# Kernel optimization log

Measured on AMD Instinct MI355X. Metric: run time of the kernel, lower is better.

## Reference

```python
import jax, jax.numpy as jnp
import numpy as np

S = 16          # slice count (init kwarg)
EPS = 1e-5      # BN2d default eps


def markov_sub(m, s):
    """Vectorized get_markov_sub. m: [C, C] -> [s, C, C].
    ms[i][a,b] = where(m[i,b] > 0, m[a,b], 0); mss[k] = max over rows i in slice k.
    Equivalent closed form via per-column any/all positivity of the slice rows."""
    C = m.shape[0]
    pos = (m > 0.0).reshape(s, C // s, C)          # [s, slice_size, C]
    any_p = pos.any(axis=1)[:, None, :]            # [s, 1, C]
    all_p = pos.all(axis=1)[:, None, :]            # [s, 1, C]
    mb = m[None, :, :]                             # [1, C, C]
    return jnp.where(all_p, mb,
                     jnp.where(any_p, jnp.maximum(mb, 0.0), jnp.zeros_like(mb)))


def setup_inputs() -> dict:
    key = jax.random.key(0)
    ks = jax.random.split(key, 8)
    N, C, H, W = 4, 256, 32, 32
    s = S
    feats = jax.random.normal(ks[0], (N, C, H, W), jnp.float32)
    adj_matrix = jax.random.normal(ks[1], (N, C, C), jnp.float32)
    # three 1x1 conv layers: in = S*C, out = C (stacked on leading axis)
    conv_w = jax.random.normal(ks[2], (3, C, s * C), jnp.float32) / np.sqrt(s * C).astype(np.float32)
    conv_b = jax.random.normal(ks[3], (3, C), jnp.float32) * 0.01
    bn_gamma = jnp.ones((3, C), jnp.float32)
    bn_beta = jnp.zeros((3, C), jnp.float32)
    bn_mean = jax.random.normal(ks[4], (3, C), jnp.float32) * 0.1
    bn_var = jax.random.uniform(ks[5], (3, C), jnp.float32, minval=0.5, maxval=1.5)
    return {"feats": feats, "adj_matrix": adj_matrix, "conv_w": conv_w,
            "conv_b": conv_b, "bn_gamma": bn_gamma, "bn_beta": bn_beta,
            "bn_mean": bn_mean, "bn_var": bn_var}


def reference(feats, adj_matrix, conv_w, conv_b, bn_gamma, bn_beta, bn_mean, bn_var):
    N, C, H, W = feats.shape
    s = S
    # per-sample markov sub-adjacencies, computed once and reused across layers
    mss = jax.vmap(lambda m: markov_sub(m, s))(adj_matrix)      # [N, S, C, C]
    mss = mss.reshape(N, s * C, C)                              # [N, S*C, C]
    outs = []
    x = feats
    for l in range(3):
        xp = x.reshape(N, C, H * W)                             # [N, C, HW]
        y = jnp.einsum('nkc,ncp->nkp', mss, xp)                 # sparse.mm -> [N, S*C, HW]
        y = jnp.einsum('ok,nkp->nop', conv_w[l], y) + conv_b[l][None, :, None]
        scale = (bn_gamma[l] * jax.lax.rsqrt(bn_var[l] + EPS))[None, :, None]
        y = (y - bn_mean[l][None, :, None]) * scale + bn_beta[l][None, :, None]
        y = jax.nn.relu(y).reshape(N, C, H, W)
        outs.append(y)
        x = y
    return tuple(outs)
```

## Files before the change

kernel.cpp:

```cpp
#include <hip/hip_runtime.h>
#include <stdint.h>

#define CC   256
#define NB   4
#define HWP  1024
#define EPSV 1e-5f

typedef __attribute__((ext_vector_type(8))) short bf16x8;
typedef __attribute__((ext_vector_type(4))) float f32x4;

__device__ __forceinline__ ushort f2bf(float f) {
    uint32_t u = __float_as_uint(f);
    uint32_t r = (u + 0x7FFFu + ((u >> 16) & 1u)) >> 16;
    return (ushort)r;
}

__global__ __launch_bounds__(256) void prep_kernel(const float* __restrict__ adj,
                                                   const float* __restrict__ conv_w,
                                                   ushort* __restrict__ mpT,
                                                   uint8_t* __restrict__ flags,
                                                   ushort* __restrict__ cwS) {
    const int t = threadIdx.x;
    if (blockIdx.x < 64) {
        const int bb = blockIdx.x;
        const int n = bb >> 4;
        const int at = (bb >> 2) & 3, bt = bb & 3;
        const int a0 = at * 64, b0 = bt * 64;
        const float* m = adj + (size_t)n * CC * CC;
        __shared__ float Ms[64][68];
        {
            const int ar = t >> 2, bq = (t & 3) * 16;
            const float* src = m + (size_t)(a0 + ar) * CC + b0 + bq;
#pragma unroll
            for (int i = 0; i < 4; ++i)
                *(float4*)&Ms[ar][bq + i * 4] = *(const float4*)(src + i * 4);
        }
        __syncthreads();
        {
            const int bl = t >> 2, ac = (t & 3) * 16;
            ushort* dst = mpT + ((size_t)n * CC + b0 + bl) * CC + a0 + ac;
#pragma unroll
            for (int a4 = 0; a4 < 4; ++a4) {
                ushort4 o;
                o.x = f2bf(fmaxf(Ms[ac + a4 * 4 + 0][bl], 0.f));
                o.y = f2bf(fmaxf(Ms[ac + a4 * 4 + 1][bl], 0.f));
                o.z = f2bf(fmaxf(Ms[ac + a4 * 4 + 2][bl], 0.f));
                o.w = f2bf(fmaxf(Ms[ac + a4 * 4 + 3][bl], 0.f));
                *(ushort4*)(dst + a4 * 4) = o;
            }
        }
        {
            const int kl = t >> 6, bl = t & 63;
            bool allp = true, anyp = false;
#pragma unroll
            for (int i = 0; i < 16; ++i) {
                bool p = Ms[kl * 16 + i][bl] > 0.0f;
                allp = allp && p;
                anyp = anyp || p;
            }
            const uint8_t f = allp ? (uint8_t)2 : (anyp ? (uint8_t)1 : (uint8_t)0);
            flags[(((size_t)n * CC) + b0 + bl) * 16 + at * 4 + kl] = f;
        }
    } else {
        const int idx = ((blockIdx.x - 64) * 256 + t) * 4;
        const float* src = conv_w + ((size_t)(idx >> 8)) * 4096 + (idx & 255);
        float4 s = {0.f, 0.f, 0.f, 0.f};
#pragma unroll
        for (int k = 0; k < 16; ++k) {
            float4 v = *(const float4*)(src + k * 256);
            s.x += v.x; s.y += v.y; s.z += v.z; s.w += v.w;
        }
        ushort4 ob = {f2bf(s.x), f2bf(s.y), f2bf(s.z), f2bf(s.w)};
        *(ushort4*)(cwS + idx) = ob;
    }
}

__global__ __launch_bounds__(256) void wbase_mfma(const ushort* __restrict__ cwS,
                                                  const ushort* __restrict__ mpT,
                                                  const uint8_t* __restrict__ flags,
                                                  const float* __restrict__ adj,
                                                  const float* __restrict__ conv_w,
                                                  const float* __restrict__ gamma,
                                                  const float* __restrict__ var,
                                                  ushort* __restrict__ Ws) {
    const int tile = blockIdx.x;
    const int ln = blockIdx.y;
    const int l = ln >> 2, n = ln & 3;
    const int trow = (tile >> 2) * 64, tcol = (tile & 3) * 64;
    const ushort* A = cwS + (size_t)l * 65536;
    const ushort* B = mpT + (size_t)n * 65536;
    __shared__ ushort Al[64][40];
    __shared__ ushort Bl[64][40];
    __shared__ int   s_badcnt;
    __shared__ int   s_bad[1024];
    __shared__ float s_v[256];
    __shared__ float s_corr[64];
    const int t = threadIdx.x;
    const int wv = t >> 6, L = t & 63;
    const int wr = (wv >> 1) * 32, wc = (wv & 1) * 32;
    const int l16 = L & 15, q = L >> 4;
    const int r0 = t >> 2, kq0 = (t & 3) * 8;
    f32x4 acc[2][2];
#pragma unroll
    for (int i = 0; i < 2; ++i)
#pragma unroll
        for (int j = 0; j < 2; ++j)
            acc[i][j] = (f32x4){0.f, 0.f, 0.f, 0.f};

    if (t == 0) s_badcnt = 0;

    for (int kt = 0; kt < 8; ++kt) {
        const int kk = kt * 32;
        int4 av = *(const int4*)(A + (size_t)(trow + r0) * CC + kk + kq0);
        int4 bv = *(const int4*)(B + (size_t)(tcol + r0) * CC + kk + kq0);
        __syncthreads();
        *(int4*)&Al[r0][kq0] = av;
        *(int4*)&Bl[r0][kq0] = bv;
        __syncthreads();
        bf16x8 af[2], bfr[2];
#pragma unroll
        for (int i = 0; i < 2; ++i)
            af[i] = *(const bf16x8*)&Al[wr + i * 16 + l16][q * 8];
#pragma unroll
        for (int j = 0; j < 2; ++j)
            bfr[j] = *(const bf16x8*)&Bl[wc + j * 16 + l16][q * 8];
#pragma unroll
        for (int i = 0; i < 2; ++i)
#pragma unroll
            for (int j = 0; j < 2; ++j)
                acc[i][j] = __builtin_amdgcn_mfma_f32_16x16x32_bf16(af[i], bfr[j], acc[i][j], 0, 0, 0);
    }

    if (t < 64) {
        const uint8_t* fb = flags + (((size_t)n * CC) + tcol + t) * 16;
        const uint4 fv = *(const uint4*)fb;
        if ((fv.x != 0x01010101u) || (fv.y != 0x01010101u) ||
            (fv.z != 0x01010101u) || (fv.w != 0x01010101u)) {
            for (int k = 0; k < 16; ++k) {
                const int f = fb[k];
                if (f != 1) {
                    int pos = atomicAdd(&s_badcnt, 1);
                    s_bad[pos] = (t << 8) | (k << 2) | f;
                }
            }
        }
    }
    __syncthreads();
    const int nbad = s_badcnt;
    for (int e = 0; e < nbad; ++e) {
        const int enc = s_bad[e];
        const int bl = enc >> 8, k = (enc >> 2) & 15, f = enc & 3;
        const int b = tcol + bl;
        {
            const float mv = adj[(size_t)n * 65536 + (size_t)t * CC + b];
            s_v[t] = (f == 0) ? fmaxf(mv, 0.f) : fmaxf(-mv, 0.f);
        }
        __syncthreads();
        {
            const float* cw = conv_w + (size_t)l * 1048576 +
                              (size_t)(trow + (t >> 2)) * 4096 + k * 256 + (t & 3) * 64;
            const float* vv = s_v + (t & 3) * 64;
            float s = 0.f;
#pragma unroll 16
            for (int a = 0; a < 64; ++a) s += cw[a] * vv[a];
            s += __shfl_xor(s, 1);
            s += __shfl_xor(s, 2);
            if ((t & 3) == 0) s_corr[t >> 2] = s;
        }
        __syncthreads();
#pragma unroll
        for (int j = 0; j < 2; ++j) {
            if (wc + j * 16 + l16 == bl) {
#pragma unroll
                for (int i = 0; i < 2; ++i)
#pragma unroll
                    for (int r = 0; r < 4; ++r)
                        acc[i][j][r] -= s_corr[wr + i * 16 + q * 4 + r];
            }
        }
        __syncthreads();
    }

    ushort* W = Ws + (size_t)ln * 65536;
#pragma unroll
    for (int i = 0; i < 2; ++i)
#pragma unroll
        for (int j = 0; j < 2; ++j) {
            const int ob = trow + wr + i * 16 + q * 4;
            const int b  = tcol + wc + j * 16 + l16;
#pragma unroll
            for (int r = 0; r < 4; ++r) {
                const int o = ob + r;
                const float sc = gamma[l * CC + o] * rsqrtf(var[l * CC + o] + EPSV);
                W[(size_t)o * CC + b] = f2bf(acc[i][j][r] * sc);
            }
        }
}

__global__ __launch_bounds__(256) void fused_layers(const float* __restrict__ feats,
                                                    const ushort* __restrict__ Ws,
                                                    const float* __restrict__ conv_b,
                                                    const float* __restrict__ gamma,
                                                    const float* __restrict__ beta,
                                                    const float* __restrict__ mean,
                                                    const float* __restrict__ var,
                                                    float* __restrict__ out) {
    const int n = blockIdx.y;
    const int p0 = blockIdx.x * 16;
    __shared__ ushort xl[2][16][264];
    const int t = threadIdx.x;
    const int wv = t >> 6, L = t & 63;
    const int l16 = L & 15, q = L >> 4;

    {
        const float* src = feats + ((size_t)n * CC + t) * HWP + p0;
        float v[16];
#pragma unroll
        for (int i = 0; i < 4; ++i)
            *(float4*)&v[i * 4] = *(const float4*)(src + i * 4);
#pragma unroll
        for (int i = 0; i < 16; ++i)
            xl[0][i][t] = f2bf(v[i]);
    }
    __syncthreads();

    int cur = 0;
    for (int l = 0; l < 3; ++l) {
        const ushort* Bw = Ws + (size_t)(l * 4 + n) * 65536;
        f32x4 acc[4];
#pragma unroll
        for (int jj = 0; jj < 4; ++jj) acc[jj] = (f32x4){0.f, 0.f, 0.f, 0.f};

#pragma unroll
        for (int kt = 0; kt < 8; ++kt) {
            const int kk = kt * 32;
            bf16x8 af = *(const bf16x8*)&xl[cur][l16][kk + q * 8];
#pragma unroll
            for (int jj = 0; jj < 4; ++jj) {
                const int o = (wv * 4 + jj) * 16 + l16;
                bf16x8 bv = *(const bf16x8*)(Bw + (size_t)o * CC + kk + q * 8);
                acc[jj] = __builtin_amdgcn_mfma_f32_16x16x32_bf16(af, bv, acc[jj], 0, 0, 0);
            }
        }

        float* outn = out + (size_t)(l * 4 + n) * CC * HWP;
#pragma unroll
        for (int jj = 0; jj < 4; ++jj) {
            const int o = (wv * 4 + jj) * 16 + l16;
            const float sc = gamma[l * CC + o] * rsqrtf(var[l * CC + o] + EPSV);
            const float b2 = sc * (conv_b[l * CC + o] - mean[l * CC + o]) + beta[l * CC + o];
            const float v0 = fmaxf(acc[jj][0] + b2, 0.f);
            const float v1 = fmaxf(acc[jj][1] + b2, 0.f);
            const float v2 = fmaxf(acc[jj][2] + b2, 0.f);
            const float v3 = fmaxf(acc[jj][3] + b2, 0.f);
            *(float4*)(outn + (size_t)o * HWP + p0 + q * 4) = (float4){v0, v1, v2, v3};
            if (l < 2) {
                xl[cur ^ 1][q * 4 + 0][o] = f2bf(v0);
                xl[cur ^ 1][q * 4 + 1][o] = f2bf(v1);
                xl[cur ^ 1][q * 4 + 2][o] = f2bf(v2);
                xl[cur ^ 1][q * 4 + 3][o] = f2bf(v3);
            }
        }
        __syncthreads();
        cur ^= 1;
    }
}

extern "C" void kernel_launch(void* const* d_in, const int* in_sizes, int n_in,
                              void* d_out, int out_size, void* d_ws, size_t ws_size,
                              hipStream_t stream) {
    const float* feats  = (const float*)d_in[0];
    const float* adj    = (const float*)d_in[1];
    const float* conv_w = (const float*)d_in[2];
    const float* conv_b = (const float*)d_in[3];
    const float* gamma  = (const float*)d_in[4];
    const float* beta   = (const float*)d_in[5];
    const float* mean   = (const float*)d_in[6];
    const float* var    = (const float*)d_in[7];
    float* out = (float*)d_out;

    char* ws = (char*)d_ws;
    uint8_t* flags = (uint8_t*)ws;
    ushort*  cwS   = (ushort*)(ws + 16384);
    ushort*  mpT   = (ushort*)(ws + 409600);
    ushort*  Wsb   = (ushort*)(ws + 933888);

    prep_kernel<<<256, 256, 0, stream>>>(adj, conv_w, mpT, flags, cwS);
    wbase_mfma<<<dim3(16, 12), 256, 0, stream>>>(cwS, mpT, flags, adj, conv_w, gamma, var, Wsb);
    fused_layers<<<dim3(64, NB), 256, 0, stream>>>(feats, Wsb, conv_b, gamma, beta, mean, var, out);
}
```

Measured before the change: 114.3 us.

## Merge three kernels into one cooperative kernel with grid-wide syncs

```diff
diff --git a/kernel.cpp b/kernel.cpp
--- a/kernel.cpp
+++ b/kernel.cpp
@@ -1,5 +1,8 @@
 #include <hip/hip_runtime.h>
+#include <hip/hip_cooperative_groups.h>
 #include <stdint.h>
+
+namespace cg = cooperative_groups;
 
 #define CC   256
 #define NB   4
@@ -15,19 +18,35 @@
     return (ushort)r;
 }
 
-__global__ __launch_bounds__(256) void prep_kernel(const float* __restrict__ adj,
-                                                   const float* __restrict__ conv_w,
-                                                   ushort* __restrict__ mpT,
-                                                   uint8_t* __restrict__ flags,
-                                                   ushort* __restrict__ cwS) {
+__global__ __launch_bounds__(256) void mega_kernel(
+    const float* __restrict__ adj,   const float* __restrict__ conv_w,
+    const float* __restrict__ feats, const float* __restrict__ conv_b,
+    const float* __restrict__ gamma, const float* __restrict__ beta,
+    const float* __restrict__ mean,  const float* __restrict__ var,
+    float* __restrict__ out,
+    uint8_t* __restrict__ flags, ushort* __restrict__ cwS,
+    ushort* __restrict__ mpT,    ushort* __restrict__ Ws) {
+    cg::grid_group grid = cg::this_grid();
     const int t = threadIdx.x;
-    if (blockIdx.x < 64) {
-        const int bb = blockIdx.x;
-        const int n = bb >> 4;
-        const int at = (bb >> 2) & 3, bt = bb & 3;
+    const int bid = blockIdx.x;
+
+    __shared__ float  Ms[64][68];
+    __shared__ ushort Al[64][40];
+    __shared__ ushort Bl[64][40];
+    __shared__ int    s_badcnt;
+    __shared__ int    s_bad[1024];
+    __shared__ float  s_v[256];
+    __shared__ float  s_corr[64];
+    __shared__ ushort xl[2][16][264];
+
+    const int wv = t >> 6, L = t & 63;
+    const int l16 = L & 15, q = L >> 4;
+
+    if (bid < 64) {
+        const int n = bid >> 4;
+        const int at = (bid >> 2) & 3, bt = bid & 3;
         const int a0 = at * 64, b0 = bt * 64;
         const float* m = adj + (size_t)n * CC * CC;
-        __shared__ float Ms[64][68];
         {
             const int ar = t >> 2, bq = (t & 3) * 16;
             const float* src = m + (size_t)(a0 + ar) * CC + b0 + bq;
@@ -62,7 +81,7 @@
             flags[(((size_t)n * CC) + b0 + bl) * 16 + at * 4 + kl] = f;
         }
     } else {
-        const int idx = ((blockIdx.x - 64) * 256 + t) * 4;
+        const int idx = ((bid - 64) * 256 + t) * 4;
         const float* src = conv_w + ((size_t)(idx >> 8)) * 4096 + (idx & 255);
         float4 s = {0.f, 0.f, 0.f, 0.f};
 #pragma unroll
@@ -73,146 +92,8 @@
         ushort4 ob = {f2bf(s.x), f2bf(s.y), f2bf(s.z), f2bf(s.w)};
         *(ushort4*)(cwS + idx) = ob;
     }
-}
-
-__global__ __launch_bounds__(256) void wbase_mfma(const ushort* __restrict__ cwS,
-                                                  const ushort* __restrict__ mpT,
-                                                  const uint8_t* __restrict__ flags,
-                                                  const float* __restrict__ adj,
-                                                  const float* __restrict__ conv_w,
-                                                  const float* __restrict__ gamma,
-                                                  const float* __restrict__ var,
-                                                  ushort* __restrict__ Ws) {
-    const int tile = blockIdx.x;
-    const int ln = blockIdx.y;
-    const int l = ln >> 2, n = ln & 3;
-    const int trow = (tile >> 2) * 64, tcol = (tile & 3) * 64;
-    const ushort* A = cwS + (size_t)l * 65536;
-    const ushort* B = mpT + (size_t)n * 65536;
-    __shared__ ushort Al[64][40];
-    __shared__ ushort Bl[64][40];
-    __shared__ int   s_badcnt;
-    __shared__ int   s_bad[1024];
-    __shared__ float s_v[256];
-    __shared__ float s_corr[64];
-    const int t = threadIdx.x;
-    const int wv = t >> 6, L = t & 63;
-    const int wr = (wv >> 1) * 32, wc = (wv & 1) * 32;
-    const int l16 = L & 15, q = L >> 4;
-    const int r0 = t >> 2, kq0 = (t & 3) * 8;
-    f32x4 acc[2][2];
-#pragma unroll
-    for (int i = 0; i < 2; ++i)
-#pragma unroll
-        for (int j = 0; j < 2; ++j)
-            acc[i][j] = (f32x4){0.f, 0.f, 0.f, 0.f};
-
-    if (t == 0) s_badcnt = 0;
-
-    for (int kt = 0; kt < 8; ++kt) {
-        const int kk = kt * 32;
-        int4 av = *(const int4*)(A + (size_t)(trow + r0) * CC + kk + kq0);
-        int4 bv = *(const int4*)(B + (size_t)(tcol + r0) * CC + kk + kq0);
-        __syncthreads();
-        *(int4*)&Al[r0][kq0] = av;
-        *(int4*)&Bl[r0][kq0] = bv;
-        __syncthreads();
-        bf16x8 af[2], bfr[2];
-#pragma unroll
-        for (int i = 0; i < 2; ++i)
-            af[i] = *(const bf16x8*)&Al[wr + i * 16 + l16][q * 8];
-#pragma unroll
-        for (int j = 0; j < 2; ++j)
-            bfr[j] = *(const bf16x8*)&Bl[wc + j * 16 + l16][q * 8];
-#pragma unroll
-        for (int i = 0; i < 2; ++i)
-#pragma unroll
-            for (int j = 0; j < 2; ++j)
-                acc[i][j] = __builtin_amdgcn_mfma_f32_16x16x32_bf16(af[i], bfr[j], acc[i][j], 0, 0, 0);
-    }
-
-    if (t < 64) {
-        const uint8_t* fb = flags + (((size_t)n * CC) + tcol + t) * 16;
-        const uint4 fv = *(const uint4*)fb;
-        if ((fv.x != 0x01010101u) || (fv.y != 0x01010101u) ||
-            (fv.z != 0x01010101u) || (fv.w != 0x01010101u)) {
-            for (int k = 0; k < 16; ++k) {
-                const int f = fb[k];
-                if (f != 1) {
-                    int pos = atomicAdd(&s_badcnt, 1);
-                    s_bad[pos] = (t << 8) | (k << 2) | f;
-                }
-            }
-        }
-    }
-    __syncthreads();
-    const int nbad = s_badcnt;
-    for (int e = 0; e < nbad; ++e) {
-        const int enc = s_bad[e];
-        const int bl = enc >> 8, k = (enc >> 2) & 15, f = enc & 3;
-        const int b = tcol + bl;
-        {
-            const float mv = adj[(size_t)n * 65536 + (size_t)t * CC + b];
-            s_v[t] = (f == 0) ? fmaxf(mv, 0.f) : fmaxf(-mv, 0.f);
-        }
-        __syncthreads();
-        {
-            const float* cw = conv_w + (size_t)l * 1048576 +
-                              (size_t)(trow + (t >> 2)) * 4096 + k * 256 + (t & 3) * 64;
-            const float* vv = s_v + (t & 3) * 64;
-            float s = 0.f;
-#pragma unroll 16
-            for (int a = 0; a < 64; ++a) s += cw[a] * vv[a];
-            s += __shfl_xor(s, 1);
-            s += __shfl_xor(s, 2);
-            if ((t & 3) == 0) s_corr[t >> 2] = s;
-        }
-        __syncthreads();
-#pragma unroll
-        for (int j = 0; j < 2; ++j) {
-            if (wc + j * 16 + l16 == bl) {
-#pragma unroll
-                for (int i = 0; i < 2; ++i)
-#pragma unroll
-                    for (int r = 0; r < 4; ++r)
-                        acc[i][j][r] -= s_corr[wr + i * 16 + q * 4 + r];
-            }
-        }
-        __syncthreads();
-    }
-
-    ushort* W = Ws + (size_t)ln * 65536;
-#pragma unroll
-    for (int i = 0; i < 2; ++i)
-#pragma unroll
-        for (int j = 0; j < 2; ++j) {
-            const int ob = trow + wr + i * 16 + q * 4;
-            const int b  = tcol + wc + j * 16 + l16;
-#pragma unroll
-            for (int r = 0; r < 4; ++r) {
-                const int o = ob + r;
-                const float sc = gamma[l * CC + o] * rsqrtf(var[l * CC + o] + EPSV);
-                W[(size_t)o * CC + b] = f2bf(acc[i][j][r] * sc);
-            }
-        }
-}
-
-__global__ __launch_bounds__(256) void fused_layers(const float* __restrict__ feats,
-                                                    const ushort* __restrict__ Ws,
-                                                    const float* __restrict__ conv_b,
-                                                    const float* __restrict__ gamma,
-                                                    const float* __restrict__ beta,
-                                                    const float* __restrict__ mean,
-                                                    const float* __restrict__ var,
-                                                    float* __restrict__ out) {
-    const int n = blockIdx.y;
-    const int p0 = blockIdx.x * 16;
-    __shared__ ushort xl[2][16][264];
-    const int t = threadIdx.x;
-    const int wv = t >> 6, L = t & 63;
-    const int l16 = L & 15, q = L >> 4;
-
     {
+        const int n = bid >> 6, p0 = (bid & 63) * 16;
         const float* src = feats + ((size_t)n * CC + t) * HWP + p0;
         float v[16];
 #pragma unroll
@@ -222,56 +103,165 @@
         for (int i = 0; i < 16; ++i)
             xl[0][i][t] = f2bf(v[i]);
     }
-    __syncthreads();
-
-    int cur = 0;
-    for (int l = 0; l < 3; ++l) {
-        const ushort* Bw = Ws + (size_t)(l * 4 + n) * 65536;
-        f32x4 acc[4];
-#pragma unroll
-        for (int jj = 0; jj < 4; ++jj) acc[jj] = (f32x4){0.f, 0.f, 0.f, 0.f};
-
-#pragma unroll
+    grid.sync();
+
+    if (bid < 192) {
+        const int tile = bid & 15, ln = bid >> 4;
+        const int l = ln >> 2, n = ln & 3;
+        const int trow = (tile >> 2) * 64, tcol = (tile & 3) * 64;
+        const ushort* A = cwS + (size_t)l * 65536;
+        const ushort* B = mpT + (size_t)n * 65536;
+        const int wr = (wv >> 1) * 32, wc = (wv & 1) * 32;
+        const int r0 = t >> 2, kq0 = (t & 3) * 8;
+        f32x4 acc[2][2];
+#pragma unroll
+        for (int i = 0; i < 2; ++i)
+#pragma unroll
+            for (int j = 0; j < 2; ++j)
+                acc[i][j] = (f32x4){0.f, 0.f, 0.f, 0.f};
+
+        if (t == 0) s_badcnt = 0;
+
         for (int kt = 0; kt < 8; ++kt) {
             const int kk = kt * 32;
-            bf16x8 af = *(const bf16x8*)&xl[cur][l16][kk + q * 8];
+            int4 av = *(const int4*)(A + (size_t)(trow + r0) * CC + kk + kq0);
+            int4 bv = *(const int4*)(B + (size_t)(tcol + r0) * CC + kk + kq0);
+            __syncthreads();
+            *(int4*)&Al[r0][kq0] = av;
+            *(int4*)&Bl[r0][kq0] = bv;
+            __syncthreads();
+            bf16x8 af[2], bfr[2];
+#pragma unroll
+            for (int i = 0; i < 2; ++i)
+                af[i] = *(const bf16x8*)&Al[wr + i * 16 + l16][q * 8];
+#pragma unroll
+            for (int j = 0; j < 2; ++j)
+                bfr[j] = *(const bf16x8*)&Bl[wc + j * 16 + l16][q * 8];
+#pragma unroll
+            for (int i = 0; i < 2; ++i)
+#pragma unroll
+                for (int j = 0; j < 2; ++j)
+                    acc[i][j] = __builtin_amdgcn_mfma_f32_16x16x32_bf16(af[i], bfr[j], acc[i][j], 0, 0, 0);
+        }
+
+        if (t < 64) {
+            const uint8_t* fb = flags + (((size_t)n * CC) + tcol + t) * 16;
+            const uint4 fv = *(const uint4*)fb;
+            if ((fv.x != 0x01010101u) || (fv.y != 0x01010101u) ||
+                (fv.z != 0x01010101u) || (fv.w != 0x01010101u)) {
+                for (int k = 0; k < 16; ++k) {
+                    const int f = fb[k];
+                    if (f != 1) {
+                        int pos = atomicAdd(&s_badcnt, 1);
+                        s_bad[pos] = (t << 8) | (k << 2) | f;
+                    }
+                }
+            }
+        }
+        __syncthreads();
+        const int nbad = s_badcnt;
+        for (int e = 0; e < nbad; ++e) {
+            const int enc = s_bad[e];
+            const int bl = enc >> 8, k = (enc >> 2) & 15, f = enc & 3;
+            const int b = tcol + bl;
+            {
+                const float mv = adj[(size_t)n * 65536 + (size_t)t * CC + b];
+                s_v[t] = (f == 0) ? fmaxf(mv, 0.f) : fmaxf(-mv, 0.f);
+            }
+            __syncthreads();
+            {
+                const float* cw = conv_w + (size_t)l * 1048576 +
+                                  (size_t)(trow + (t >> 2)) * 4096 + k * 256 + (t & 3) * 64;
+                const float* vv = s_v + (t & 3) * 64;
+                float s = 0.f;
+#pragma unroll 16
+                for (int a = 0; a < 64; ++a) s += cw[a] * vv[a];
+                s += __shfl_xor(s, 1);
+                s += __shfl_xor(s, 2);
+                if ((t & 3) == 0) s_corr[t >> 2] = s;
+            }
+            __syncthreads();
+#pragma unroll
+            for (int j = 0; j < 2; ++j) {
+                if (wc + j * 16 + l16 == bl) {
+#pragma unroll
+                    for (int i = 0; i < 2; ++i)
+#pragma unroll
+                        for (int r = 0; r < 4; ++r)
+                            acc[i][j][r] -= s_corr[wr + i * 16 + q * 4 + r];
+                }
+            }
+            __syncthreads();
+        }
+
+        ushort* W = Ws + (size_t)ln * 65536;
+#pragma unroll
+        for (int i = 0; i < 2; ++i)
+#pragma unroll
+            for (int j = 0; j < 2; ++j) {
+                const int ob = trow + wr + i * 16 + q * 4;
+                const int b  = tcol + wc + j * 16 + l16;
+#pragma unroll
+                for (int r = 0; r < 4; ++r) {
+                    const int o = ob + r;
+                    const float sc = gamma[l * CC + o] * rsqrtf(var[l * CC + o] + EPSV);
+                    W[(size_t)o * CC + b] = f2bf(acc[i][j][r] * sc);
+                }
+            }
+    }
+    grid.sync();
+
+    {
+        const int n = bid >> 6, p0 = (bid & 63) * 16;
+        int cur = 0;
+        for (int l = 0; l < 3; ++l) {
+            const ushort* Bw = Ws + (size_t)(l * 4 + n) * 65536;
+            f32x4 acc[4];
+#pragma unroll
+            for (int jj = 0; jj < 4; ++jj) acc[jj] = (f32x4){0.f, 0.f, 0.f, 0.f};
+
+#pragma unroll
+            for (int kt = 0; kt < 8; ++kt) {
+                const int kk = kt * 32;
+                bf16x8 af = *(const bf16x8*)&xl[cur][l16][kk + q * 8];
+#pragma unroll
+                for (int jj = 0; jj < 4; ++jj) {
+                    const int o = (wv * 4 + jj) * 16 + l16;
+                    bf16x8 bv = *(const bf16x8*)(Bw + (size_t)o * CC + kk + q * 8);
+                    acc[jj] = __builtin_amdgcn_mfma_f32_16x16x32_bf16(af, bv, acc[jj], 0, 0, 0);
+                }
+            }
+
+            float* outn = out + (size_t)(l * 4 + n) * CC * HWP;
 #pragma unroll
             for (int jj = 0; jj < 4; ++jj) {
                 const int o = (wv * 4 + jj) * 16 + l16;
-                bf16x8 bv = *(const bf16x8*)(Bw + (size_t)o * CC + kk + q * 8);
-                acc[jj] = __builtin_amdgcn_mfma_f32_16x16x32_bf16(af, bv, acc[jj], 0, 0, 0);
-            }
-        }
-
-        float* outn = out + (size_t)(l * 4 + n) * CC * HWP;
-#pragma unroll
-        for (int jj = 0; jj < 4; ++jj) {
-            const int o = (wv * 4 + jj) * 16 + l16;
-            const float sc = gamma[l * CC + o] * rsqrtf(var[l * CC + o] + EPSV);
-            const float b2 = sc * (conv_b[l * CC + o] - mean[l * CC + o]) + beta[l * CC + o];
-            const float v0 = fmaxf(acc[jj][0] + b2, 0.f);
-            const float v1 = fmaxf(acc[jj][1] + b2, 0.f);
-            const float v2 = fmaxf(acc[jj][2] + b2, 0.f);
-            const float v3 = fmaxf(acc[jj][3] + b2, 0.f);
-            *(float4*)(outn + (size_t)o * HWP + p0 + q * 4) = (float4){v0, v1, v2, v3};
-            if (l < 2) {
-                xl[cur ^ 1][q * 4 + 0][o] = f2bf(v0);
-                xl[cur ^ 1][q * 4 + 1][o] = f2bf(v1);
-                xl[cur ^ 1][q * 4 + 2][o] = f2bf(v2);
-                xl[cur ^ 1][q * 4 + 3][o] = f2bf(v3);
-            }
-        }
-        __syncthreads();
-        cur ^= 1;
+                const float sc = gamma[l * CC + o] * rsqrtf(var[l * CC + o] + EPSV);
+                const float b2 = sc * (conv_b[l * CC + o] - mean[l * CC + o]) + beta[l * CC + o];
+                const float v0 = fmaxf(acc[jj][0] + b2, 0.f);
+                const float v1 = fmaxf(acc[jj][1] + b2, 0.f);
+                const float v2 = fmaxf(acc[jj][2] + b2, 0.f);
+                const float v3 = fmaxf(acc[jj][3] + b2, 0.f);
+                *(float4*)(outn + (size_t)o * HWP + p0 + q * 4) = (float4){v0, v1, v2, v3};
+                if (l < 2) {
+                    xl[cur ^ 1][q * 4 + 0][o] = f2bf(v0);
+                    xl[cur ^ 1][q * 4 + 1][o] = f2bf(v1);
+                    xl[cur ^ 1][q * 4 + 2][o] = f2bf(v2);
+                    xl[cur ^ 1][q * 4 + 3][o] = f2bf(v3);
+                }
+            }
+            __syncthreads();
+            cur ^= 1;
+        }
     }
 }
 
 extern "C" void kernel_launch(void* const* d_in, const int* in_sizes, int n_in,
                               void* d_out, int out_size, void* d_ws, size_t ws_size,
                               hipStream_t stream) {
-    const float* feats  = (const float*)d_in[0];
     const float* adj    = (const float*)d_in[1];
     const float* conv_w = (const float*)d_in[2];
+    const float* feats  = (const float*)d_in[0];
     const float* conv_b = (const float*)d_in[3];
     const float* gamma  = (const float*)d_in[4];
     const float* beta   = (const float*)d_in[5];
@@ -285,7 +275,8 @@
     ushort*  mpT   = (ushort*)(ws + 409600);
     ushort*  Wsb   = (ushort*)(ws + 933888);
 
-    prep_kernel<<<256, 256, 0, stream>>>(adj, conv_w, mpT, flags, cwS);
-    wbase_mfma<<<dim3(16, 12), 256, 0, stream>>>(cwS, mpT, flags, adj, conv_w, gamma, var, Wsb);
-    fused_layers<<<dim3(64, NB), 256, 0, stream>>>(feats, Wsb, conv_b, gamma, beta, mean, var, out);
+    void* args[] = {(void*)&adj, (void*)&conv_w, (void*)&feats, (void*)&conv_b,
+                    (void*)&gamma, (void*)&beta, (void*)&mean, (void*)&var,
+                    (void*)&out, (void*)&flags, (void*)&cwS, (void*)&mpT, (void*)&Wsb};
+    hipLaunchCooperativeKernel((void*)mega_kernel, dim3(256), dim3(256), args, 0, stream);
 }
```

Measured after the change: 173.2 us. 51.5% more time.

## Stage wbase K in two 128-wide halves and widen fused_layers to 512 threads

Applied to the files above, without the earlier changes.

```diff
diff --git a/kernel.cpp b/kernel.cpp
--- a/kernel.cpp
+++ b/kernel.cpp
@@ -89,8 +89,8 @@
     const int trow = (tile >> 2) * 64, tcol = (tile & 3) * 64;
     const ushort* A = cwS + (size_t)l * 65536;
     const ushort* B = mpT + (size_t)n * 65536;
-    __shared__ ushort Al[64][40];
-    __shared__ ushort Bl[64][40];
+    __shared__ ushort Al[64][130];
+    __shared__ ushort Bl[64][130];
     __shared__ int   s_badcnt;
     __shared__ int   s_bad[1024];
     __shared__ float s_v[256];
@@ -99,7 +99,7 @@
     const int wv = t >> 6, L = t & 63;
     const int wr = (wv >> 1) * 32, wc = (wv & 1) * 32;
     const int l16 = L & 15, q = L >> 4;
-    const int r0 = t >> 2, kq0 = (t & 3) * 8;
+    const int lr = t >> 2, lc0 = (t & 3) * 32;
     f32x4 acc[2][2];
 #pragma unroll
     for (int i = 0; i < 2; ++i)
@@ -109,21 +109,54 @@
 
     if (t == 0) s_badcnt = 0;
 
-    for (int kt = 0; kt < 8; ++kt) {
-        const int kk = kt * 32;
-        int4 av = *(const int4*)(A + (size_t)(trow + r0) * CC + kk + kq0);
-        int4 bv = *(const int4*)(B + (size_t)(tcol + r0) * CC + kk + kq0);
-        __syncthreads();
-        *(int4*)&Al[r0][kq0] = av;
-        *(int4*)&Bl[r0][kq0] = bv;
-        __syncthreads();
+    const ushort* Arow = A + (size_t)(trow + lr) * CC + lc0;
+    const ushort* Brow = B + (size_t)(tcol + lr) * CC + lc0;
+    int4 a1[4], b1[4], a2[4], b2[4];
+#pragma unroll
+    for (int j = 0; j < 4; ++j) a1[j] = *(const int4*)(Arow + j * 8);
+#pragma unroll
+    for (int j = 0; j < 4; ++j) b1[j] = *(const int4*)(Brow + j * 8);
+#pragma unroll
+    for (int j = 0; j < 4; ++j) {
+        *(int4*)&Al[lr][lc0 + j * 8] = a1[j];
+        *(int4*)&Bl[lr][lc0 + j * 8] = b1[j];
+    }
+    __syncthreads();
+#pragma unroll
+    for (int j = 0; j < 4; ++j) a2[j] = *(const int4*)(Arow + 128 + j * 8);
+#pragma unroll
+    for (int j = 0; j < 4; ++j) b2[j] = *(const int4*)(Brow + 128 + j * 8);
+#pragma unroll
+    for (int ktl = 0; ktl < 4; ++ktl) {
         bf16x8 af[2], bfr[2];
 #pragma unroll
         for (int i = 0; i < 2; ++i)
-            af[i] = *(const bf16x8*)&Al[wr + i * 16 + l16][q * 8];
+            af[i] = *(const bf16x8*)&Al[wr + i * 16 + l16][ktl * 32 + q * 8];
 #pragma unroll
         for (int j = 0; j < 2; ++j)
-            bfr[j] = *(const bf16x8*)&Bl[wc + j * 16 + l16][q * 8];
+            bfr[j] = *(const bf16x8*)&Bl[wc + j * 16 + l16][ktl * 32 + q * 8];
+#pragma unroll
+        for (int i = 0; i < 2; ++i)
+#pragma unroll
+            for (int j = 0; j < 2; ++j)
+                acc[i][j] = __builtin_amdgcn_mfma_f32_16x16x32_bf16(af[i], bfr[j], acc[i][j], 0, 0, 0);
+    }
+    __syncthreads();
+#pragma unroll
+    for (int j = 0; j < 4; ++j) {
+        *(int4*)&Al[lr][lc0 + j * 8] = a2[j];
+        *(int4*)&Bl[lr][lc0 + j * 8] = b2[j];
+    }
+    __syncthreads();
+#pragma unroll
+    for (int ktl = 0; ktl < 4; ++ktl) {
+        bf16x8 af[2], bfr[2];
+#pragma unroll
+        for (int i = 0; i < 2; ++i)
+            af[i] = *(const bf16x8*)&Al[wr + i * 16 + l16][ktl * 32 + q * 8];
+#pragma unroll
+        for (int j = 0; j < 2; ++j)
+            bfr[j] = *(const bf16x8*)&Bl[wc + j * 16 + l16][ktl * 32 + q * 8];
 #pragma unroll
         for (int i = 0; i < 2; ++i)
 #pragma unroll
@@ -197,7 +230,7 @@
         }
 }
 
-__global__ __launch_bounds__(256) void fused_layers(const float* __restrict__ feats,
+__global__ __launch_bounds__(512) void fused_layers(const float* __restrict__ feats,
                                                     const ushort* __restrict__ Ws,
                                                     const float* __restrict__ conv_b,
                                                     const float* __restrict__ gamma,
@@ -213,31 +246,32 @@
     const int l16 = L & 15, q = L >> 4;
 
     {
-        const float* src = feats + ((size_t)n * CC + t) * HWP + p0;
-        float v[16];
-#pragma unroll
-        for (int i = 0; i < 4; ++i)
+        const int c = t >> 1, h = t & 1;
+        const float* src = feats + ((size_t)n * CC + c) * HWP + p0 + h * 8;
+        float v[8];
+#pragma unroll
+        for (int i = 0; i < 2; ++i)
             *(float4*)&v[i * 4] = *(const float4*)(src + i * 4);
 #pragma unroll
-        for (int i = 0; i < 16; ++i)
-            xl[0][i][t] = f2bf(v[i]);
+        for (int i = 0; i < 8; ++i)
+            xl[0][h * 8 + i][c] = f2bf(v[i]);
     }
     __syncthreads();
 
     int cur = 0;
     for (int l = 0; l < 3; ++l) {
         const ushort* Bw = Ws + (size_t)(l * 4 + n) * 65536;
-        f32x4 acc[4];
-#pragma unroll
-        for (int jj = 0; jj < 4; ++jj) acc[jj] = (f32x4){0.f, 0.f, 0.f, 0.f};
+        f32x4 acc[2];
+#pragma unroll
+        for (int jj = 0; jj < 2; ++jj) acc[jj] = (f32x4){0.f, 0.f, 0.f, 0.f};
 
 #pragma unroll
         for (int kt = 0; kt < 8; ++kt) {
             const int kk = kt * 32;
             bf16x8 af = *(const bf16x8*)&xl[cur][l16][kk + q * 8];
 #pragma unroll
-            for (int jj = 0; jj < 4; ++jj) {
-                const int o = (wv * 4 + jj) * 16 + l16;
+            for (int jj = 0; jj < 2; ++jj) {
+                const int o = (wv * 2 + jj) * 16 + l16;
                 bf16x8 bv = *(const bf16x8*)(Bw + (size_t)o * CC + kk + q * 8);
                 acc[jj] = __builtin_amdgcn_mfma_f32_16x16x32_bf16(af, bv, acc[jj], 0, 0, 0);
             }
@@ -245,8 +279,8 @@
 
         float* outn = out + (size_t)(l * 4 + n) * CC * HWP;
 #pragma unroll
-        for (int jj = 0; jj < 4; ++jj) {
-            const int o = (wv * 4 + jj) * 16 + l16;
+        for (int jj = 0; jj < 2; ++jj) {
+            const int o = (wv * 2 + jj) * 16 + l16;
             const float sc = gamma[l * CC + o] * rsqrtf(var[l * CC + o] + EPSV);
             const float b2 = sc * (conv_b[l * CC + o] - mean[l * CC + o]) + beta[l * CC + o];
             const float v0 = fmaxf(acc[jj][0] + b2, 0.f);
@@ -287,5 +321,5 @@
 
     prep_kernel<<<256, 256, 0, stream>>>(adj, conv_w, mpT, flags, cwS);
     wbase_mfma<<<dim3(16, 12), 256, 0, stream>>>(cwS, mpT, flags, adj, conv_w, gamma, var, Wsb);
-    fused_layers<<<dim3(64, NB), 256, 0, stream>>>(feats, Wsb, conv_b, gamma, beta, mean, var, out);
-}
+    fused_layers<<<dim3(64, NB), 512, 0, stream>>>(feats, Wsb, conv_b, gamma, beta, mean, var, out);
+}
```

Result: faster. 109.3 us (-4.4%).

## Drop LDS staging in weight GEMM and double threads in fused layers kernel

Applied to the files above, without the earlier changes.

```diff
diff --git a/kernel.cpp b/kernel.cpp
--- a/kernel.cpp
+++ b/kernel.cpp
@@ -89,8 +89,6 @@
     const int trow = (tile >> 2) * 64, tcol = (tile & 3) * 64;
     const ushort* A = cwS + (size_t)l * 65536;
     const ushort* B = mpT + (size_t)n * 65536;
-    __shared__ ushort Al[64][40];
-    __shared__ ushort Bl[64][40];
     __shared__ int   s_badcnt;
     __shared__ int   s_bad[1024];
     __shared__ float s_v[256];
@@ -99,7 +97,6 @@
     const int wv = t >> 6, L = t & 63;
     const int wr = (wv >> 1) * 32, wc = (wv & 1) * 32;
     const int l16 = L & 15, q = L >> 4;
-    const int r0 = t >> 2, kq0 = (t & 3) * 8;
     f32x4 acc[2][2];
 #pragma unroll
     for (int i = 0; i < 2; ++i)
@@ -109,26 +106,21 @@
 
     if (t == 0) s_badcnt = 0;
 
+    const ushort* Ar0 = A + (size_t)(trow + wr + l16) * CC + q * 8;
+    const ushort* Ar1 = Ar0 + (size_t)16 * CC;
+    const ushort* Br0 = B + (size_t)(tcol + wc + l16) * CC + q * 8;
+    const ushort* Br1 = Br0 + (size_t)16 * CC;
+#pragma unroll
     for (int kt = 0; kt < 8; ++kt) {
         const int kk = kt * 32;
-        int4 av = *(const int4*)(A + (size_t)(trow + r0) * CC + kk + kq0);
-        int4 bv = *(const int4*)(B + (size_t)(tcol + r0) * CC + kk + kq0);
-        __syncthreads();
-        *(int4*)&Al[r0][kq0] = av;
-        *(int4*)&Bl[r0][kq0] = bv;
-        __syncthreads();
-        bf16x8 af[2], bfr[2];
-#pragma unroll
-        for (int i = 0; i < 2; ++i)
-            af[i] = *(const bf16x8*)&Al[wr + i * 16 + l16][q * 8];
-#pragma unroll
-        for (int j = 0; j < 2; ++j)
-            bfr[j] = *(const bf16x8*)&Bl[wc + j * 16 + l16][q * 8];
-#pragma unroll
-        for (int i = 0; i < 2; ++i)
-#pragma unroll
-            for (int j = 0; j < 2; ++j)
-                acc[i][j] = __builtin_amdgcn_mfma_f32_16x16x32_bf16(af[i], bfr[j], acc[i][j], 0, 0, 0);
+        bf16x8 af0 = *(const bf16x8*)(Ar0 + kk);
+        bf16x8 af1 = *(const bf16x8*)(Ar1 + kk);
+        bf16x8 bf0 = *(const bf16x8*)(Br0 + kk);
+        bf16x8 bf1 = *(const bf16x8*)(Br1 + kk);
+        acc[0][0] = __builtin_amdgcn_mfma_f32_16x16x32_bf16(af0, bf0, acc[0][0], 0, 0, 0);
+        acc[0][1] = __builtin_amdgcn_mfma_f32_16x16x32_bf16(af0, bf1, acc[0][1], 0, 0, 0);
+        acc[1][0] = __builtin_amdgcn_mfma_f32_16x16x32_bf16(af1, bf0, acc[1][0], 0, 0, 0);
+        acc[1][1] = __builtin_amdgcn_mfma_f32_16x16x32_bf16(af1, bf1, acc[1][1], 0, 0, 0);
     }
 
     if (t < 64) {
@@ -197,7 +189,7 @@
         }
 }
 
-__global__ __launch_bounds__(256) void fused_layers(const float* __restrict__ feats,
+__global__ __launch_bounds__(512) void fused_layers(const float* __restrict__ feats,
                                                     const ushort* __restrict__ Ws,
                                                     const float* __restrict__ conv_b,
                                                     const float* __restrict__ gamma,
@@ -213,31 +205,32 @@
     const int l16 = L & 15, q = L >> 4;
 
     {
-        const float* src = feats + ((size_t)n * CC + t) * HWP + p0;
-        float v[16];
-#pragma unroll
-        for (int i = 0; i < 4; ++i)
+        const int c = t >> 1, h = t & 1;
+        const float* src = feats + ((size_t)n * CC + c) * HWP + p0 + h * 8;
+        float v[8];
+#pragma unroll
+        for (int i = 0; i < 2; ++i)
             *(float4*)&v[i * 4] = *(const float4*)(src + i * 4);
 #pragma unroll
-        for (int i = 0; i < 16; ++i)
-            xl[0][i][t] = f2bf(v[i]);
+        for (int i = 0; i < 8; ++i)
+            xl[0][h * 8 + i][c] = f2bf(v[i]);
     }
     __syncthreads();
 
     int cur = 0;
     for (int l = 0; l < 3; ++l) {
         const ushort* Bw = Ws + (size_t)(l * 4 + n) * 65536;
-        f32x4 acc[4];
-#pragma unroll
-        for (int jj = 0; jj < 4; ++jj) acc[jj] = (f32x4){0.f, 0.f, 0.f, 0.f};
+        f32x4 acc[2];
+#pragma unroll
+        for (int jj = 0; jj < 2; ++jj) acc[jj] = (f32x4){0.f, 0.f, 0.f, 0.f};
 
 #pragma unroll
         for (int kt = 0; kt < 8; ++kt) {
             const int kk = kt * 32;
             bf16x8 af = *(const bf16x8*)&xl[cur][l16][kk + q * 8];
 #pragma unroll
-            for (int jj = 0; jj < 4; ++jj) {
-                const int o = (wv * 4 + jj) * 16 + l16;
+            for (int jj = 0; jj < 2; ++jj) {
+                const int o = (wv * 2 + jj) * 16 + l16;
                 bf16x8 bv = *(const bf16x8*)(Bw + (size_t)o * CC + kk + q * 8);
                 acc[jj] = __builtin_amdgcn_mfma_f32_16x16x32_bf16(af, bv, acc[jj], 0, 0, 0);
             }
@@ -245,8 +238,8 @@
 
         float* outn = out + (size_t)(l * 4 + n) * CC * HWP;
 #pragma unroll
-        for (int jj = 0; jj < 4; ++jj) {
-            const int o = (wv * 4 + jj) * 16 + l16;
+        for (int jj = 0; jj < 2; ++jj) {
+            const int o = (wv * 2 + jj) * 16 + l16;
             const float sc = gamma[l * CC + o] * rsqrtf(var[l * CC + o] + EPSV);
             const float b2 = sc * (conv_b[l * CC + o] - mean[l * CC + o]) + beta[l * CC + o];
             const float v0 = fmaxf(acc[jj][0] + b2, 0.f);
@@ -287,5 +280,5 @@
 
     prep_kernel<<<256, 256, 0, stream>>>(adj, conv_w, mpT, flags, cwS);
     wbase_mfma<<<dim3(16, 12), 256, 0, stream>>>(cwS, mpT, flags, adj, conv_w, gamma, var, Wsb);
-    fused_layers<<<dim3(64, NB), 256, 0, stream>>>(feats, Wsb, conv_b, gamma, beta, mean, var, out);
-}
+    fused_layers<<<dim3(64, NB), 512, 0, stream>>>(feats, Wsb, conv_b, gamma, beta, mean, var, out);
+}
```

Result: faster. 105.6 us (-7.7%).
